# Kernel optimization log

Measured on AMD Instinct MI355X. Metric: run time of the kernel, lower is better.

## Reference

```python
import jax, jax.numpy as jnp
import numpy as np

N, E_DIM, H, N_EDGES, OUT = 4096, 256, 4, 131072, 256


def _ln(x, g, b, eps=1e-5):
    m = x.mean(-1, keepdims=True)
    v = ((x - m) ** 2).mean(-1, keepdims=True)
    return (x - m) / jnp.sqrt(v + eps) * g + b


def _mha(q_in, kv_in, in_w, in_b, out_w, out_b, n_heads):
    # torch nn.MultiheadAttention with packed in_proj_weight [3E, E]
    e = q_in.shape[-1]
    dh = e // n_heads
    wq, wk, wv = jnp.split(in_w, 3, axis=0)
    bq, bk, bv = jnp.split(in_b, 3)
    q = (q_in @ wq.T + bq).reshape(-1, n_heads, dh)   # [N,H,Dh]
    k = (kv_in @ wk.T + bk).reshape(-1, n_heads, dh)
    v = (kv_in @ wv.T + bv).reshape(-1, n_heads, dh)
    scale = 1.0 / jnp.sqrt(jnp.asarray(dh, q.dtype))
    scores = jnp.einsum('nhd,mhd->hnm', q, k) * scale  # [H,N,M]
    attn = jax.nn.softmax(scores, axis=-1)
    o = jnp.einsum('hnm,mhd->nhd', attn, v).reshape(-1, e)
    return o @ out_w.T + out_b


def _gcn_conv(x, edge_index):
    # out[c] += (1/sqrt(d[c])) * (1/sqrt(d[r])) * x[r] for each edge (r,c),
    # d = in-degree counted on col; non-finite norms zeroed (nan_to_num)
    n = x.shape[0]
    row, col = edge_index[0], edge_index[1]
    d = jax.ops.segment_sum(jnp.ones_like(col, dtype=x.dtype), col, num_segments=n)
    dn = 1.0 / jnp.sqrt(d)
    value = dn[col] * dn[row]
    value = jnp.where(jnp.isfinite(value), value, 0.0)
    return jax.ops.segment_sum(value[:, None] * x[row], col, num_segments=n)


def setup_inputs() -> dict:
    key = jax.random.key(0)
    ks = jax.random.split(key, 12)
    s = 1.0 / np.sqrt(E_DIM)
    rn = lambda k, shape: jax.random.normal(k, shape, jnp.float32) * s
    return {
        'x': jax.random.normal(ks[0], (N, E_DIM), jnp.float32),
        'edge_index': jax.random.randint(ks[1], (2, N_EDGES), 0, N, dtype=jnp.int32),
        'weight_local': jax.random.uniform(ks[2], (E_DIM, E_DIM), jnp.float32, -s, s),
        'sa_in_w': rn(ks[3], (3 * E_DIM, E_DIM)),
        'sa_in_b': jnp.zeros((3 * E_DIM,), jnp.float32),
        'sa_out_w': rn(ks[4], (E_DIM, E_DIM)),
        'sa_out_b': jnp.zeros((E_DIM,), jnp.float32),
        'ln1_g': jnp.ones((E_DIM,), jnp.float32),
        'ln1_b': jnp.zeros((E_DIM,), jnp.float32),
        'ca_in_w': rn(ks[5], (3 * E_DIM, E_DIM)),
        'ca_in_b': jnp.zeros((3 * E_DIM,), jnp.float32),
        'ca_out_w': rn(ks[6], (E_DIM, E_DIM)),
        'ca_out_b': jnp.zeros((E_DIM,), jnp.float32),
        'ln2_g': jnp.ones((E_DIM,), jnp.float32),
        'ln2_b': jnp.zeros((E_DIM,), jnp.float32),
        'gate_w': rn(ks[7], (E_DIM, 2 * E_DIM)),
        'gate_b': jnp.zeros((E_DIM,), jnp.float32),
        'fc_w': rn(ks[8], (OUT, E_DIM)),
        'fc_b': jnp.zeros((OUT,), jnp.float32),
    }


def reference(x, edge_index, weight_local, sa_in_w, sa_in_b, sa_out_w, sa_out_b,
              ln1_g, ln1_b, ca_in_w, ca_in_b, ca_out_w, ca_out_b, ln2_g, ln2_b,
              gate_w, gate_b, fc_w, fc_b):
    hi = _gcn_conv(x, edge_index)                       # [N,E]
    local_embed = hi @ weight_local                     # [N,E]
    attn_out = _mha(x, x, sa_in_w, sa_in_b, sa_out_w, sa_out_b, H)
    global_embed = _ln(x + attn_out, ln1_g, ln1_b)      # [N,E]
    cross_out = _mha(global_embed, local_embed, ca_in_w, ca_in_b, ca_out_w, ca_out_b, H)
    aligned = _ln(global_embed + cross_out, ln2_g, ln2_b)
    concat = jnp.concatenate([global_embed, aligned], axis=-1)  # [N,2E]
    final_embed = jax.nn.relu(concat @ gate_w.T + gate_b)
    return final_embed @ fc_w.T + fc_b
```

## Files before the change

kernel.cpp:

```cpp
#include <hip/hip_runtime.h>
#include <hip/hip_bf16.h>

#define NN 4096
#define EDIM 256
#define NHEAD 4
#define DH 64
#define NEDGE 131072
#define NE (NN * EDIM)
#define NSPLIT 8
#define KEYS_PER_SPLIT (NN / NSPLIT)

typedef __bf16 bf16x8 __attribute__((ext_vector_type(8)));
typedef float f32x4 __attribute__((ext_vector_type(4)));
typedef float f32x16 __attribute__((ext_vector_type(16)));

__device__ inline void gload_lds16(const void* g, void* l) {
    __builtin_amdgcn_global_load_lds((const __attribute__((address_space(1))) unsigned int*)g,
                                     (__attribute__((address_space(3))) unsigned int*)l, 16, 0, 0);
}

__global__ __launch_bounds__(256) void prep_kernel(
    const float* __restrict__ wl, const float* __restrict__ siw, const float* __restrict__ sib,
    const float* __restrict__ sow, const float* __restrict__ ciw, const float* __restrict__ cib,
    const float* __restrict__ cow, const float* __restrict__ gw, const float* __restrict__ fw,
    const float* __restrict__ x,
    __bf16* __restrict__ siwb, __bf16* __restrict__ ciwb, __bf16* __restrict__ sowb,
    __bf16* __restrict__ cowb, __bf16* __restrict__ gwb, __bf16* __restrict__ fwb,
    __bf16* __restrict__ wlT, __bf16* __restrict__ xb,
    float* __restrict__ sib_adj, float* __restrict__ cib_adj) {
    long i = (long)blockIdx.x * 256 + threadIdx.x;
    if (i < 196608) { float v = siw[i]; if (i < 65536) v *= 0.125f; siwb[i] = (__bf16)v; return; }
    i -= 196608;
    if (i < 196608) { float v = ciw[i]; if (i < 65536) v *= 0.125f; ciwb[i] = (__bf16)v; return; }
    i -= 196608;
    if (i < 65536) { sowb[i] = (__bf16)sow[i]; return; }
    i -= 65536;
    if (i < 65536) { cowb[i] = (__bf16)cow[i]; return; }
    i -= 65536;
    if (i < 131072) { gwb[i] = (__bf16)gw[i]; return; }
    i -= 131072;
    if (i < 65536) { fwb[i] = (__bf16)fw[i]; return; }
    i -= 65536;
    if (i < 65536) { int n = (int)(i >> 8), k = (int)(i & 255); wlT[i] = (__bf16)wl[k * 256 + n]; return; }
    i -= 65536;
    if (i < 1048576) { xb[i] = (__bf16)x[i]; return; }
    i -= 1048576;
    if (i < 768) { sib_adj[i] = sib[i] * (i < 256 ? 0.125f : 1.f); return; }
    i -= 768;
    if (i < 768) { cib_adj[i] = cib[i] * (i < 256 ? 0.125f : 1.f); return; }
}

__global__ __launch_bounds__(256) void degi_kernel(const int* __restrict__ ei,
                                                   int* __restrict__ degi, int ne) {
    int e = blockIdx.x * 256 + threadIdx.x;
    if (e < ne) atomicAdd(&degi[ei[ne + e]], 1);
}

__global__ __launch_bounds__(256) void scan_kernel(const int* __restrict__ degi,
                                                   int* __restrict__ off,
                                                   int* __restrict__ cursor,
                                                   float* __restrict__ dnz) {
    __shared__ int s[256];
    const int t = threadIdx.x, i0 = t * 16;
    int v[16], sum = 0;
#pragma unroll
    for (int j = 0; j < 16; ++j) { v[j] = degi[i0 + j]; sum += v[j]; }
    s[t] = sum;
    __syncthreads();
#pragma unroll
    for (int d = 1; d < 256; d <<= 1) {
        int add = (t >= d) ? s[t - d] : 0;
        __syncthreads();
        s[t] += add;
        __syncthreads();
    }
    int base = s[t] - sum;
#pragma unroll
    for (int j = 0; j < 16; ++j) {
        off[i0 + j] = base;
        cursor[i0 + j] = base;
        dnz[i0 + j] = (v[j] > 0) ? rsqrtf((float)v[j]) : 0.f;
        base += v[j];
    }
}

__global__ __launch_bounds__(256) void fill_kernel(const int* __restrict__ ei,
                                                   int* __restrict__ cursor,
                                                   int* __restrict__ rows, int ne) {
    int e = blockIdx.x * 256 + threadIdx.x;
    if (e < ne) {
        int r = ei[e], c = ei[ne + e];
        int pos = atomicAdd(&cursor[c], 1);
        rows[pos] = r;
    }
}

__global__ __launch_bounds__(256) void gather_kernel(const int* __restrict__ off,
                                                     const int* __restrict__ rows,
                                                     const float* __restrict__ dnz,
                                                     const float* __restrict__ x,
                                                     __bf16* __restrict__ hib) {
    const int c = blockIdx.x, t = threadIdx.x;
    const int s0 = off[c];
    const int s1 = (c == NN - 1) ? NEDGE : off[c + 1];
    float acc = 0.f;
    for (int j = s0; j < s1; ++j) {
        int r = rows[j];
        acc += dnz[r] * x[(size_t)r * EDIM + t];
    }
    hib[(size_t)c * EDIM + t] = (__bf16)(dnz[c] * acc);
}

template <bool RELU, bool OUTBF>
__global__ __launch_bounds__(256) void gemm_bf16(const __bf16* __restrict__ A,
                                                 const __bf16* __restrict__ A2, int lda,
                                                 const __bf16* __restrict__ Bt, int ldb,
                                                 const float* __restrict__ bias,
                                                 void* __restrict__ Cv, int ldc, int K) {
    __shared__ __align__(16) __bf16 As[4096];
    __shared__ __align__(16) __bf16 Bs[4096];
    const int tid = threadIdx.x;
    const int row0 = blockIdx.y * 64, col0 = blockIdx.x * 64;
    const int w = tid >> 6, l = tid & 63, lr = l & 15, lk = l >> 4;
    f32x4 acc[4] = {};

    for (int k0 = 0; k0 < K; k0 += 64) {
        if (k0) __syncthreads();
        const __bf16* Asrc = A;
        int ka = k0;
        if (A2 != nullptr && k0 >= 256) { Asrc = A2; ka = k0 - 256; }
#pragma unroll
        for (int cc = 0; cc < 2; ++cc) {
            int E0 = (w * 2 + cc) * 512;
            int row = (E0 >> 6) + (l >> 3);
            int col = (l & 7) * 8;
            int sc = col ^ ((row & 7) << 3);
            gload_lds16(Asrc + (size_t)(row0 + row) * lda + ka + sc, &As[E0]);
            gload_lds16(Bt + (size_t)(col0 + row) * ldb + k0 + sc, &Bs[E0]);
        }
        __syncthreads();
#pragma unroll
        for (int ks = 0; ks < 2; ++ks) {
            int cswz = (ks * 32 + lk * 8) ^ ((lr & 7) << 3);
            bf16x8 af = *(bf16x8*)&As[(w * 16 + lr) * 64 + cswz];
#pragma unroll
            for (int nt = 0; nt < 4; ++nt) {
                bf16x8 bfr = *(bf16x8*)&Bs[(nt * 16 + lr) * 64 + cswz];
                acc[nt] = __builtin_amdgcn_mfma_f32_16x16x32_bf16(af, bfr, acc[nt], 0, 0, 0);
            }
        }
    }
#pragma unroll
    for (int nt = 0; nt < 4; ++nt) {
        float bv = bias ? bias[col0 + nt * 16 + lr] : 0.f;
#pragma unroll
        for (int r = 0; r < 4; ++r) {
            float v = acc[nt][r] + bv;
            if (RELU) v = fmaxf(v, 0.f);
            size_t ci = (size_t)(row0 + w * 16 + lk * 4 + r) * ldc + col0 + nt * 16 + lr;
            if (OUTBF) ((__bf16*)Cv)[ci] = (__bf16)v;
            else ((float*)Cv)[ci] = v;
        }
    }
}

__global__ __launch_bounds__(256) void transpose_v(const __bf16* __restrict__ qkvb,
                                                   __bf16* __restrict__ Vtb) {
    const int h = blockIdx.y, n0 = blockIdx.x * 64;
    __shared__ __bf16 Vs[64][65];
    const int tid = threadIdx.x;
    {
        int row = tid >> 2, c0 = (tid & 3) * 16;
        const __bf16* vp = &qkvb[(size_t)(n0 + row) * 768 + 512 + h * 64 + c0];
        bf16x8 v0 = *(const bf16x8*)vp;
        bf16x8 v1 = *(const bf16x8*)(vp + 8);
#pragma unroll
        for (int i = 0; i < 8; ++i) Vs[row][c0 + i] = v0[i];
#pragma unroll
        for (int i = 0; i < 8; ++i) Vs[row][c0 + 8 + i] = v1[i];
    }
    __syncthreads();
    int d = tid >> 2, j0 = (tid & 3) * 16;
    bf16x8 o0, o1;
#pragma unroll
    for (int i = 0; i < 8; ++i) o0[i] = Vs[j0 + i][d];
#pragma unroll
    for (int i = 0; i < 8; ++i) o1[i] = Vs[j0 + 8 + i][d];
    __bf16* dst = &Vtb[((size_t)h * 64 + d) * NN + n0 + j0];
    *(bf16x8*)dst = o0;
    *(bf16x8*)(dst + 8) = o1;
}

__global__ __launch_bounds__(256, 4) void attn_split(const __bf16* __restrict__ qkvb,
                                                     const __bf16* __restrict__ Vtb,
                                                     __bf16* __restrict__ p0,
                                                     __bf16* __restrict__ p1,
                                                     __bf16* __restrict__ p2,
                                                     __bf16* __restrict__ p3,
                                                     float* __restrict__ ml) {
    const int h = blockIdx.y, s = blockIdx.z;
    const int n0 = blockIdx.x * 128;
    const int tid = threadIdx.x;
    const int w = tid >> 6, l = tid & 63;
    const int qi = l & 31, hi = l >> 5, hi8 = hi * 8;
    const int swz = (l & 7) << 3;

    __shared__ __align__(16) __bf16 Kt[4096];
    __shared__ __align__(16) __bf16 Vt[4096];

    const int qrow = n0 + w * 32 + qi;
    bf16x8 qf[4];
#pragma unroll
    for (int d0 = 0; d0 < 4; ++d0)
        qf[d0] = *(const bf16x8*)&qkvb[(size_t)qrow * 768 + h * 64 + d0 * 16 + hi8];

    f32x16 ot0 = {}, ot1 = {};
    float sum_part = 0.f;
    const __bf16* Vbh = Vtb + (size_t)h * 64 * NN;

    for (int t = 0; t < KEYS_PER_SPLIT / 64; ++t) {
        const int kv0 = s * KEYS_PER_SPLIT + t * 64;
        __syncthreads();
#pragma unroll
        for (int cc = 0; cc < 2; ++cc) {
            int E0 = (w * 2 + cc) * 512;
            int row = (E0 >> 6) + (l >> 3);
            int col = (l & 7) * 8;
            int sc = col ^ ((row & 7) << 3);
            gload_lds16(qkvb + (size_t)(kv0 + row) * 768 + 256 + h * 64 + sc, &Kt[E0]);
            gload_lds16(Vbh + (size_t)row * NN + kv0 + sc, &Vt[E0]);
        }
        __syncthreads();

#pragma unroll
        for (int ss = 0; ss < 2; ++ss) {
            f32x16 st = {};
#pragma unroll
            for (int d0 = 0; d0 < 4; ++d0) {
                bf16x8 kf = *(bf16x8*)&Kt[(ss * 32 + qi) * 64 + ((d0 * 16 + hi8) ^ swz)];
                st = __builtin_amdgcn_mfma_f32_32x32x16_bf16(kf, qf[d0], st, 0, 0, 0);
            }
            float p_[16];
#pragma unroll
            for (int r = 0; r < 16; ++r) {
                p_[r] = __expf(fminf(st[r], 30.f));
                sum_part += p_[r];
            }
            unsigned int wd[8];
#pragma unroll
            for (int j = 0; j < 8; ++j)
                asm("v_cvt_pk_bf16_f32 %0, %1, %2" : "=v"(wd[j]) : "v"(p_[2 * j]), "v"(p_[2 * j + 1]));
            asm("v_permlane32_swap_b32 %0, %1" : "+v"(wd[0]), "+v"(wd[2]));
            asm("v_permlane32_swap_b32 %0, %1" : "+v"(wd[1]), "+v"(wd[3]));
            asm("v_permlane32_swap_b32 %0, %1" : "+v"(wd[4]), "+v"(wd[6]));
            asm("v_permlane32_swap_b32 %0, %1" : "+v"(wd[5]), "+v"(wd[7]));
            union { unsigned int u[4]; bf16x8 v; } pa0, pa1;
            pa0.u[0] = wd[0]; pa0.u[1] = wd[1]; pa0.u[2] = wd[2]; pa0.u[3] = wd[3];
            pa1.u[0] = wd[4]; pa1.u[1] = wd[5]; pa1.u[2] = wd[6]; pa1.u[3] = wd[7];
#pragma unroll
            for (int kt = 0; kt < 2; ++kt) {
                bf16x8 pav = kt ? pa1.v : pa0.v;
                int colk = (ss * 32 + kt * 16 + hi8) ^ swz;
                bf16x8 vf0 = *(bf16x8*)&Vt[qi * 64 + colk];
                bf16x8 vf1 = *(bf16x8*)&Vt[(32 + qi) * 64 + colk];
                ot0 = __builtin_amdgcn_mfma_f32_32x32x16_bf16(vf0, pav, ot0, 0, 0, 0);
                ot1 = __builtin_amdgcn_mfma_f32_32x32x16_bf16(vf1, pav, ot1, 0, 0, 0);
            }
        }
    }

    float tot = sum_part + __shfl_xor(sum_part, 32);
    __bf16* pb;
    switch (s >> 1) {
        case 0: pb = p0; break;
        case 1: pb = p1; break;
        case 2: pb = p2; break;
        default: pb = p3; break;
    }
    pb += (size_t)(s & 1) * NN * 256;
    __bf16* dst = &pb[(size_t)qrow * 256 + h * 64];
#pragma unroll
    for (int r = 0; r < 16; r += 2) {
        int d = (r & 3) + 8 * (r >> 2) + 4 * hi;
        union { unsigned int u; __bf16 b[2]; } w2;
        w2.b[0] = (__bf16)ot0[r]; w2.b[1] = (__bf16)ot0[r + 1];
        *(unsigned int*)&dst[d] = w2.u;
        union { unsigned int u; __bf16 b[2]; } w3;
        w3.b[0] = (__bf16)ot1[r]; w3.b[1] = (__bf16)ot1[r + 1];
        *(unsigned int*)&dst[32 + d] = w3.u;
    }
    if (hi == 0) ml[((size_t)s * NHEAD + h) * NN + qrow] = tot;
}

__global__ __launch_bounds__(256) void attn_merge(const __bf16* __restrict__ p0,
                                                  const __bf16* __restrict__ p1,
                                                  const __bf16* __restrict__ p2,
                                                  const __bf16* __restrict__ p3,
                                                  const float* __restrict__ ml,
                                                  __bf16* __restrict__ coreb) {
    int idx = blockIdx.x * 256 + threadIdx.x;
    int n = idx >> 8, c = idx & 255, h = c >> 6;
    float L = 0.f, O = 0.f;
#pragma unroll
    for (int s = 0; s < NSPLIT; ++s) {
        const __bf16* pb = (s < 2 ? p0 : s < 4 ? p1 : s < 6 ? p2 : p3) + (size_t)(s & 1) * NN * 256;
        O += (float)pb[(size_t)n * 256 + c];
        L += ml[((size_t)s * NHEAD + h) * NN + n];
    }
    coreb[idx] = (__bf16)(O / L);
}

__device__ inline float block_sum256(float v, float* tmp) {
#pragma unroll
    for (int o = 32; o; o >>= 1) v += __shfl_xor(v, o);
    __syncthreads();
    if ((threadIdx.x & 63) == 0) tmp[threadIdx.x >> 6] = v;
    __syncthreads();
    return tmp[0] + tmp[1] + tmp[2] + tmp[3];
}

__global__ __launch_bounds__(256) void ln_kernel(const float* __restrict__ a,
                                                 const float* __restrict__ b,
                                                 const float* __restrict__ g,
                                                 const float* __restrict__ be,
                                                 float* __restrict__ outf,
                                                 __bf16* __restrict__ outb) {
    __shared__ float tmp[4];
    const int n = blockIdx.x, t = threadIdx.x;
    float v = a[n * EDIM + t] + b[n * EDIM + t];
    float mean = block_sum256(v, tmp) * (1.f / 256.f);
    float c = v - mean;
    float var = block_sum256(c * c, tmp) * (1.f / 256.f);
    float o = c * (1.f / sqrtf(var + 1e-5f)) * g[t] + be[t];
    if (outf) outf[n * EDIM + t] = o;
    if (outb) outb[n * EDIM + t] = (__bf16)o;
}

extern "C" void kernel_launch(void* const* d_in, const int* in_sizes, int n_in,
                              void* d_out, int out_size, void* d_ws, size_t ws_size,
                              hipStream_t stream) {
    const float* x = (const float*)d_in[0];
    const int* ei = (const int*)d_in[1];
    const float* w_local = (const float*)d_in[2];
    const float* sa_in_w = (const float*)d_in[3];
    const float* sa_in_b = (const float*)d_in[4];
    const float* sa_out_w = (const float*)d_in[5];
    const float* sa_out_b = (const float*)d_in[6];
    const float* ln1_g = (const float*)d_in[7];
    const float* ln1_b = (const float*)d_in[8];
    const float* ca_in_w = (const float*)d_in[9];
    const float* ca_in_b = (const float*)d_in[10];
    const float* ca_out_w = (const float*)d_in[11];
    const float* ca_out_b = (const float*)d_in[12];
    const float* ln2_g = (const float*)d_in[13];
    const float* ln2_b = (const float*)d_in[14];
    const float* gate_w = (const float*)d_in[15];
    const float* gate_b = (const float*)d_in[16];
    const float* fc_w = (const float*)d_in[17];
    const float* fc_b = (const float*)d_in[18];
    float* out = (float*)d_out;

    float* ws = (float*)d_ws;
    float* dnz = ws;
    float* ml = ws + 4096;
    __bf16* x_bf = (__bf16*)(ml + 131072);
    __bf16* hi_bf = (__bf16*)((float*)x_bf + NE / 2);
    __bf16* local_bf = (__bf16*)((float*)hi_bf + NE / 2);
    __bf16* qkv_bf = (__bf16*)((float*)local_bf + NE / 2);
    __bf16* core_bf = (__bf16*)((float*)qkv_bf + 3 * NE / 2);
    float* proj = (float*)core_bf + NE / 2;
    float* global_f = proj + NE;
    __bf16* global_bf = (__bf16*)(global_f + NE);
    __bf16* aligned_bf = (__bf16*)((float*)global_bf + NE / 2);
    __bf16* fin_bf = (__bf16*)((float*)aligned_bf + NE / 2);
    __bf16* vtb = (__bf16*)((float*)fin_bf + NE / 2);
    __bf16* siwb = (__bf16*)((float*)vtb + NE / 2);
    __bf16* ciwb = siwb + 196608;
    __bf16* sowb = ciwb + 196608;
    __bf16* cowb = sowb + 65536;
    __bf16* gwb = cowb + 65536;
    __bf16* fwb = gwb + 131072;
    __bf16* wlT = fwb + 65536;
    float* sib_adj = (float*)(wlT + 65536);
    float* cib_adj = sib_adj + 768;

    int* degi = (int*)qkv_bf;
    int* off = degi + 4096;
    int* cursor = off + 4096;
    int* rows = cursor + 4096;

    __bf16* pA = (__bf16*)out;
    __bf16* pB = x_bf;
    __bf16* pC = (__bf16*)proj;
    __bf16* pD = aligned_bf;

    prep_kernel<<<7174, 256, 0, stream>>>(w_local, sa_in_w, sa_in_b, sa_out_w,
                                          ca_in_w, ca_in_b, ca_out_w, gate_w, fc_w, x,
                                          siwb, ciwb, sowb, cowb, gwb, fwb, wlT, x_bf,
                                          sib_adj, cib_adj);

    hipMemsetAsync(degi, 0, 4096 * sizeof(int), stream);
    degi_kernel<<<NEDGE / 256, 256, 0, stream>>>(ei, degi, NEDGE);
    scan_kernel<<<1, 256, 0, stream>>>(degi, off, cursor, dnz);
    fill_kernel<<<NEDGE / 256, 256, 0, stream>>>(ei, cursor, rows, NEDGE);
    gather_kernel<<<NN, 256, 0, stream>>>(off, rows, dnz, x, hi_bf);

    gemm_bf16<false, true><<<dim3(4, 64), 256, 0, stream>>>(
        hi_bf, nullptr, 256, wlT, 256, nullptr, local_bf, 256, 256);

    gemm_bf16<false, true><<<dim3(12, 64), 256, 0, stream>>>(
        x_bf, nullptr, 256, siwb, 256, sib_adj, qkv_bf, 768, 256);
    transpose_v<<<dim3(64, NHEAD), 256, 0, stream>>>(qkv_bf, vtb);
    attn_split<<<dim3(NN / 128, NHEAD, NSPLIT), 256, 0, stream>>>(qkv_bf, vtb, pA, pB, pC, pD, ml);
    attn_merge<<<4096, 256, 0, stream>>>(pA, pB, pC, pD, ml, core_bf);
    gemm_bf16<false, false><<<dim3(4, 64), 256, 0, stream>>>(
        core_bf, nullptr, 256, sowb, 256, sa_out_b, proj, 256, 256);
    ln_kernel<<<NN, 256, 0, stream>>>(x, proj, ln1_g, ln1_b, global_f, global_bf);

    gemm_bf16<false, true><<<dim3(4, 64), 256, 0, stream>>>(
        global_bf, nullptr, 256, ciwb, 256, cib_adj, qkv_bf, 768, 256);
    gemm_bf16<false, true><<<dim3(8, 64), 256, 0, stream>>>(
        local_bf, nullptr, 256, ciwb + 256 * 256, 256, cib_adj + 256, qkv_bf + 256, 768, 256);
    transpose_v<<<dim3(64, NHEAD), 256, 0, stream>>>(qkv_bf, vtb);
    attn_split<<<dim3(NN / 128, NHEAD, NSPLIT), 256, 0, stream>>>(qkv_bf, vtb, pA, pB, pC, pD, ml);
    attn_merge<<<4096, 256, 0, stream>>>(pA, pB, pC, pD, ml, core_bf);
    gemm_bf16<false, false><<<dim3(4, 64), 256, 0, stream>>>(
        core_bf, nullptr, 256, cowb, 256, ca_out_b, proj, 256, 256);
    ln_kernel<<<NN, 256, 0, stream>>>(global_f, proj, ln2_g, ln2_b, nullptr, aligned_bf);

    gemm_bf16<true, true><<<dim3(4, 64), 256, 0, stream>>>(
        global_bf, aligned_bf, 256, gwb, 512, gate_b, fin_bf, 256, 512);
    gemm_bf16<false, false><<<dim3(4, 64), 256, 0, stream>>>(
        fin_bf, nullptr, 256, fwb, 256, fc_b, out, 256, 256);
}
```

Before: 192.3 us.

## Fuse local GEMM with QKV projection and write V transposed in epilogue

Merges the local-embedding GEMM and the self-attention QKV projection into one launch, and the two cross-attention projections into another. Both GEMM epilogues now write V directly into the transposed layout, which removes the separate transpose kernels and narrows the QKV buffer stride to 512. The GCN gather now reads bf16 x and splits each node's edge list across two half-blocks, halving gather bandwidth. In exchange the V stores are strided 8-byte writes, and the GCN input is rounded to bf16 before aggregation, which slightly reduces precision.

```diff
diff --git a/kernel.cpp b/kernel.cpp
--- a/kernel.cpp
+++ b/kernel.cpp
@@ -9,6 +9,7 @@
 #define NE (NN * EDIM)
 #define NSPLIT 8
 #define KEYS_PER_SPLIT (NN / NSPLIT)
+#define QKS 512
 
 typedef __bf16 bf16x8 __attribute__((ext_vector_type(8)));
 typedef float f32x4 __attribute__((ext_vector_type(4)));
@@ -98,17 +99,56 @@
 __global__ __launch_bounds__(256) void gather_kernel(const int* __restrict__ off,
                                                      const int* __restrict__ rows,
                                                      const float* __restrict__ dnz,
-                                                     const float* __restrict__ x,
+                                                     const __bf16* __restrict__ xb,
                                                      __bf16* __restrict__ hib) {
+    __shared__ float sm[2][256];
     const int c = blockIdx.x, t = threadIdx.x;
+    const int half = t >> 7, c2 = (t & 127) * 2;
     const int s0 = off[c];
     const int s1 = (c == NN - 1) ? NEDGE : off[c + 1];
-    float acc = 0.f;
-    for (int j = s0; j < s1; ++j) {
+    float a0 = 0.f, a1 = 0.f;
+    for (int j = s0 + half; j < s1; j += 2) {
         int r = rows[j];
-        acc += dnz[r] * x[(size_t)r * EDIM + t];
-    }
-    hib[(size_t)c * EDIM + t] = (__bf16)(dnz[c] * acc);
+        float dv = dnz[r];
+        unsigned int pk = *(const unsigned int*)&xb[(size_t)r * EDIM + c2];
+        a0 += dv * __uint_as_float(pk << 16);
+        a1 += dv * __uint_as_float(pk & 0xffff0000u);
+    }
+    sm[half][c2] = a0;
+    sm[half][c2 + 1] = a1;
+    __syncthreads();
+    float v = (sm[0][t] + sm[1][t]) * dnz[c];
+    hib[(size_t)c * EDIM + t] = (__bf16)v;
+}
+
+__device__ inline void gemm_core(const __bf16* __restrict__ A, int lda,
+                                 const __bf16* __restrict__ Bt, int ldb,
+                                 int row0, int col0, int K, int tid,
+                                 __bf16* As, __bf16* Bs, f32x4 acc[4]) {
+    const int w = tid >> 6, l = tid & 63, lr = l & 15, lk = l >> 4;
+    for (int k0 = 0; k0 < K; k0 += 64) {
+        if (k0) __syncthreads();
+#pragma unroll
+        for (int cc = 0; cc < 2; ++cc) {
+            int E0 = (w * 2 + cc) * 512;
+            int row = (E0 >> 6) + (l >> 3);
+            int col = (l & 7) * 8;
+            int sc = col ^ ((row & 7) << 3);
+            gload_lds16(A + (size_t)(row0 + row) * lda + k0 + sc, &As[E0]);
+            gload_lds16(Bt + (size_t)(col0 + row) * ldb + k0 + sc, &Bs[E0]);
+        }
+        __syncthreads();
+#pragma unroll
+        for (int ks = 0; ks < 2; ++ks) {
+            int cswz = (ks * 32 + lk * 8) ^ ((lr & 7) << 3);
+            bf16x8 af = *(bf16x8*)&As[(w * 16 + lr) * 64 + cswz];
+#pragma unroll
+            for (int nt = 0; nt < 4; ++nt) {
+                bf16x8 bfr = *(bf16x8*)&Bs[(nt * 16 + lr) * 64 + cswz];
+                acc[nt] = __builtin_amdgcn_mfma_f32_16x16x32_bf16(af, bfr, acc[nt], 0, 0, 0);
+            }
+        }
+    }
 }
 
 template <bool RELU, bool OUTBF>
@@ -123,7 +163,6 @@
     const int row0 = blockIdx.y * 64, col0 = blockIdx.x * 64;
     const int w = tid >> 6, l = tid & 63, lr = l & 15, lk = l >> 4;
     f32x4 acc[4] = {};
-
     for (int k0 = 0; k0 < K; k0 += 64) {
         if (k0) __syncthreads();
         const __bf16* Asrc = A;
@@ -164,31 +203,72 @@
     }
 }
 
-__global__ __launch_bounds__(256) void transpose_v(const __bf16* __restrict__ qkvb,
-                                                   __bf16* __restrict__ Vtb) {
-    const int h = blockIdx.y, n0 = blockIdx.x * 64;
-    __shared__ __bf16 Vs[64][65];
+__device__ inline void qkv_epilogue(f32x4 acc[4], const float* __restrict__ bias,
+                                    int gcol0, int row0, int tid,
+                                    __bf16* __restrict__ qkv, __bf16* __restrict__ vtb) {
+    const int w = tid >> 6, l = tid & 63, lr = l & 15, lk = l >> 4;
+    if (gcol0 < 512) {
+#pragma unroll
+        for (int nt = 0; nt < 4; ++nt) {
+            float bv = bias[gcol0 + nt * 16 + lr];
+#pragma unroll
+            for (int r = 0; r < 4; ++r)
+                qkv[(size_t)(row0 + w * 16 + lk * 4 + r) * QKS + gcol0 + nt * 16 + lr] =
+                    (__bf16)(acc[nt][r] + bv);
+        }
+    } else {
+        const int n4 = row0 + w * 16 + lk * 4;
+#pragma unroll
+        for (int nt = 0; nt < 4; ++nt) {
+            int dg = gcol0 - 512 + nt * 16 + lr;
+            float bv = bias[gcol0 + nt * 16 + lr];
+            union { __bf16 b[4]; ushort4 u; } pk;
+#pragma unroll
+            for (int r = 0; r < 4; ++r) pk.b[r] = (__bf16)(acc[nt][r] + bv);
+            *(ushort4*)&vtb[(size_t)dg * NN + n4] = pk.u;
+        }
+    }
+}
+
+__global__ __launch_bounds__(256) void fused_local_qkv(
+    const __bf16* __restrict__ hi_bf, const __bf16* __restrict__ x_bf,
+    const __bf16* __restrict__ wlT, const __bf16* __restrict__ siwb,
+    const float* __restrict__ sib,
+    __bf16* __restrict__ local_bf, __bf16* __restrict__ qkv, __bf16* __restrict__ vtb) {
+    __shared__ __align__(16) __bf16 As[4096];
+    __shared__ __align__(16) __bf16 Bs[4096];
     const int tid = threadIdx.x;
-    {
-        int row = tid >> 2, c0 = (tid & 3) * 16;
-        const __bf16* vp = &qkvb[(size_t)(n0 + row) * 768 + 512 + h * 64 + c0];
-        bf16x8 v0 = *(const bf16x8*)vp;
-        bf16x8 v1 = *(const bf16x8*)(vp + 8);
-#pragma unroll
-        for (int i = 0; i < 8; ++i) Vs[row][c0 + i] = v0[i];
-#pragma unroll
-        for (int i = 0; i < 8; ++i) Vs[row][c0 + 8 + i] = v1[i];
-    }
-    __syncthreads();
-    int d = tid >> 2, j0 = (tid & 3) * 16;
-    bf16x8 o0, o1;
-#pragma unroll
-    for (int i = 0; i < 8; ++i) o0[i] = Vs[j0 + i][d];
-#pragma unroll
-    for (int i = 0; i < 8; ++i) o1[i] = Vs[j0 + 8 + i][d];
-    __bf16* dst = &Vtb[((size_t)h * 64 + d) * NN + n0 + j0];
-    *(bf16x8*)dst = o0;
-    *(bf16x8*)(dst + 8) = o1;
+    const int bx = blockIdx.x, row0 = blockIdx.y * 64;
+    f32x4 acc[4] = {};
+    if (bx < 4) {
+        gemm_core(hi_bf, 256, wlT, 256, row0, bx * 64, 256, tid, As, Bs, acc);
+        const int w = tid >> 6, l = tid & 63, lr = l & 15, lk = l >> 4;
+#pragma unroll
+        for (int nt = 0; nt < 4; ++nt)
+#pragma unroll
+            for (int r = 0; r < 4; ++r)
+                local_bf[(size_t)(row0 + w * 16 + lk * 4 + r) * 256 + bx * 64 + nt * 16 + lr] =
+                    (__bf16)acc[nt][r];
+    } else {
+        const int gcol0 = (bx - 4) * 64;
+        gemm_core(x_bf, 256, siwb, 256, row0, gcol0, 256, tid, As, Bs, acc);
+        qkv_epilogue(acc, sib, gcol0, row0, tid, qkv, vtb);
+    }
+}
+
+__global__ __launch_bounds__(256) void fused_cross_proj(
+    const __bf16* __restrict__ global_bf, const __bf16* __restrict__ local_bf,
+    const __bf16* __restrict__ ciwb, const float* __restrict__ cib,
+    __bf16* __restrict__ qkv, __bf16* __restrict__ vtb) {
+    __shared__ __align__(16) __bf16 As[4096];
+    __shared__ __align__(16) __bf16 Bs[4096];
+    const int tid = threadIdx.x;
+    const int bx = blockIdx.x, row0 = blockIdx.y * 64;
+    const int gcol0 = (bx < 4) ? bx * 64 : 256 + (bx - 4) * 64;
+    const __bf16* A = (bx < 4) ? global_bf : local_bf;
+    f32x4 acc[4] = {};
+    gemm_core(A, 256, ciwb, 256, row0, gcol0, 256, tid, As, Bs, acc);
+    qkv_epilogue(acc, cib, gcol0, row0, tid, qkv, vtb);
 }
 
 __global__ __launch_bounds__(256, 4) void attn_split(const __bf16* __restrict__ qkvb,
@@ -212,7 +292,7 @@
     bf16x8 qf[4];
 #pragma unroll
     for (int d0 = 0; d0 < 4; ++d0)
-        qf[d0] = *(const bf16x8*)&qkvb[(size_t)qrow * 768 + h * 64 + d0 * 16 + hi8];
+        qf[d0] = *(const bf16x8*)&qkvb[(size_t)qrow * QKS + h * 64 + d0 * 16 + hi8];
 
     f32x16 ot0 = {}, ot1 = {};
     float sum_part = 0.f;
@@ -227,7 +307,7 @@
             int row = (E0 >> 6) + (l >> 3);
             int col = (l & 7) * 8;
             int sc = col ^ ((row & 7) << 3);
-            gload_lds16(qkvb + (size_t)(kv0 + row) * 768 + 256 + h * 64 + sc, &Kt[E0]);
+            gload_lds16(qkvb + (size_t)(kv0 + row) * QKS + 256 + h * 64 + sc, &Kt[E0]);
             gload_lds16(Vbh + (size_t)row * NN + kv0 + sc, &Vt[E0]);
         }
         __syncthreads();
@@ -403,25 +483,18 @@
     degi_kernel<<<NEDGE / 256, 256, 0, stream>>>(ei, degi, NEDGE);
     scan_kernel<<<1, 256, 0, stream>>>(degi, off, cursor, dnz);
     fill_kernel<<<NEDGE / 256, 256, 0, stream>>>(ei, cursor, rows, NEDGE);
-    gather_kernel<<<NN, 256, 0, stream>>>(off, rows, dnz, x, hi_bf);
-
-    gemm_bf16<false, true><<<dim3(4, 64), 256, 0, stream>>>(
-        hi_bf, nullptr, 256, wlT, 256, nullptr, local_bf, 256, 256);
-
-    gemm_bf16<false, true><<<dim3(12, 64), 256, 0, stream>>>(
-        x_bf, nullptr, 256, siwb, 256, sib_adj, qkv_bf, 768, 256);
-    transpose_v<<<dim3(64, NHEAD), 256, 0, stream>>>(qkv_bf, vtb);
+    gather_kernel<<<NN, 256, 0, stream>>>(off, rows, dnz, x_bf, hi_bf);
+
+    fused_local_qkv<<<dim3(16, 64), 256, 0, stream>>>(
+        hi_bf, x_bf, wlT, siwb, sib_adj, local_bf, qkv_bf, vtb);
     attn_split<<<dim3(NN / 128, NHEAD, NSPLIT), 256, 0, stream>>>(qkv_bf, vtb, pA, pB, pC, pD, ml);
     attn_merge<<<4096, 256, 0, stream>>>(pA, pB, pC, pD, ml, core_bf);
     gemm_bf16<false, false><<<dim3(4, 64), 256, 0, stream>>>(
         core_bf, nullptr, 256, sowb, 256, sa_out_b, proj, 256, 256);
     ln_kernel<<<NN, 256, 0, stream>>>(x, proj, ln1_g, ln1_b, global_f, global_bf);
 
-    gemm_bf16<false, true><<<dim3(4, 64), 256, 0, stream>>>(
-        global_bf, nullptr, 256, ciwb, 256, cib_adj, qkv_bf, 768, 256);
-    gemm_bf16<false, true><<<dim3(8, 64), 256, 0, stream>>>(
-        local_bf, nullptr, 256, ciwb + 256 * 256, 256, cib_adj + 256, qkv_bf + 256, 768, 256);
-    transpose_v<<<dim3(64, NHEAD), 256, 0, stream>>>(qkv_bf, vtb);
+    fused_cross_proj<<<dim3(12, 64), 256, 0, stream>>>(
+        global_bf, local_bf, ciwb, cib_adj, qkv_bf, vtb);
     attn_split<<<dim3(NN / 128, NHEAD, NSPLIT), 256, 0, stream>>>(qkv_bf, vtb, pA, pB, pC, pD, ml);
     attn_merge<<<4096, 256, 0, stream>>>(pA, pB, pC, pD, ml, core_bf);
     gemm_bf16<false, false><<<dim3(4, 64), 256, 0, stream>>>(
```

Measured after the change: 174.9 us. 1.1x faster.
